# Kernel tuning notes

Measured on AMD Instinct MI355X. Metric: run time of the kernel, lower is better.

The kernel has to match this reference:

```python
import jax, jax.numpy as jnp
import numpy as np

B, T, D = 16, 2048, 384
BLOCK = 3
NB = D // BLOCK
EPS = 1e-8


def setup_inputs() -> dict:
    key = jax.random.key(0)
    ks = jax.random.split(key, 8)
    std = 0.02
    quat_sequence = jax.random.normal(ks[0], (B, T, 4), dtype=jnp.float32)
    # weights stored as (in, out); x @ W
    W_in = jax.random.normal(ks[1], (4, D), dtype=jnp.float32) * std
    W_biv = jax.random.normal(ks[2], (D, NB * 3), dtype=jnp.float32) * (1.0 / np.sqrt(D))
    b_biv = jnp.zeros((NB * 3,), dtype=jnp.float32)
    W_dec = jax.random.normal(ks[3], (D, D), dtype=jnp.float32) * (1.0 / np.sqrt(D))
    b_dec = jnp.full((D,), 1.4, dtype=jnp.float32)
    W_inj = jax.random.normal(ks[4], (D, D), dtype=jnp.float32) * (1.0 / np.sqrt(D))
    b_inj = jax.random.normal(ks[5], (D,), dtype=jnp.float32) * (1.0 / np.sqrt(D))
    W_out = jax.random.normal(ks[6], (D, 4), dtype=jnp.float32) * std
    return {
        'quat_sequence': quat_sequence,
        'W_in': W_in, 'W_biv': W_biv, 'b_biv': b_biv,
        'W_dec': W_dec, 'b_dec': b_dec, 'W_inj': W_inj, 'b_inj': b_inj,
        'W_out': W_out,
    }


def _quat_rotate_blocks(h_blocks, bivectors):
    # h_blocks, bivectors: (..., NB, 3)
    norm_b = jnp.clip(jnp.linalg.norm(bivectors, axis=-1, keepdims=True), EPS, None)
    half = norm_b / 2
    w = jnp.cos(half)[..., 0]
    s = (jnp.sin(half) / norm_b)[..., 0]
    qx = s * bivectors[..., 2]
    qy = -s * bivectors[..., 1]
    qz = s * bivectors[..., 0]
    vx, vy, vz = h_blocks[..., 0], h_blocks[..., 1], h_blocks[..., 2]
    tx = 2 * (qy * vz - qz * vy)
    ty = 2 * (qz * vx - qx * vz)
    tz = 2 * (qx * vy - qy * vx)
    rx = vx + w * tx + (qy * tz - qz * ty)
    ry = vy + w * ty + (qz * tx - qx * tz)
    rz = vz + w * tz + (qx * ty - qy * tx)
    return jnp.stack([rx, ry, rz], axis=-1)


def reference(quat_sequence, W_in, W_biv, b_biv, W_dec, b_dec, W_inj, b_inj, W_out):
    hidden_input = quat_sequence @ W_in                       # (B,T,D)
    bivectors_all = (hidden_input @ W_biv + b_biv).reshape(B, T, NB, 3)
    decay_all = jax.nn.sigmoid(hidden_input @ W_dec + b_dec)  # (B,T,D)
    injection_all = hidden_input @ W_inj + b_inj              # (B,T,D)

    def step(h, xs):
        biv, dec, inj = xs  # (B,NB,3), (B,D), (B,D)
        rot = _quat_rotate_blocks(h.reshape(B, NB, 3), biv).reshape(B, D)
        h_next = dec * rot + inj
        return h_next, h_next

    h0 = jnp.zeros((B, D), dtype=quat_sequence.dtype)
    xs = (jnp.swapaxes(bivectors_all, 0, 1),
          jnp.swapaxes(decay_all, 0, 1),
          jnp.swapaxes(injection_all, 0, 1))
    _, hidden_seq = jax.lax.scan(step, h0, xs)                # (T,B,D)
    hidden_output = jnp.swapaxes(hidden_seq, 0, 1)            # (B,T,D)

    predicted_raw = hidden_output @ W_out                     # (B,T,4)
    norm = jnp.clip(jnp.linalg.norm(predicted_raw, axis=-1, keepdims=True), EPS, None)
    return predicted_raw / norm
```

## Files before the change

kernel.cpp:

```cpp
#include <hip/hip_runtime.h>
#include <hip/hip_bf16.h>
#include <hip/hip_fp16.h>

#define BB 16
#define TT 2048
#define DD 384
#define GG 2048
#define CC 256
#define LL 8
#define HSTRIDE (DD + 8)
#define EPSF 1e-8f
#define RCPF(x) __builtin_amdgcn_rcpf(x)


__global__ __launch_bounds__(256) void precompute_wc(
        const float* __restrict__ W_in,
        const float* __restrict__ W_biv,
        const float* __restrict__ W_dec,
        const float* __restrict__ W_inj,
        const float* __restrict__ b_biv,
        const float* __restrict__ b_dec,
        const float* __restrict__ b_inj,
        float* __restrict__ Wc) {
    int m = blockIdx.x;
    int jl = threadIdx.x & 15;
    int dp = threadIdx.x >> 4;
    int j = blockIdx.y * 16 + jl;
    const float* __restrict__ W = (m == 0) ? W_biv : (m == 1) ? W_dec : W_inj;
    float a[4] = {0.f, 0.f, 0.f, 0.f};
    for (int d = dp; d < DD; d += 16) {
        float wv = W[d * DD + j];
#pragma unroll
        for (int k = 0; k < 4; ++k) a[k] = fmaf(W_in[k * DD + d], wv, a[k]);
    }
    __shared__ float red[16][17][4];
#pragma unroll
    for (int k = 0; k < 4; ++k) red[dp][jl][k] = a[k];
    __syncthreads();
    for (int s = 8; s >= 1; s >>= 1) {
        if (dp < s) {
#pragma unroll
            for (int k = 0; k < 4; ++k) red[dp][jl][k] += red[dp + s][jl][k];
        }
        __syncthreads();
    }
    int n = j / 3, comp = j - 3 * n;
    if (dp < 4) {
        Wc[((m * 4 + dp) * 128 + n) * 4 + comp] = red[0][jl][dp];
    } else if (dp == 4) {
#pragma unroll
        for (int k = 0; k < 4; ++k) Wc[((m * 4 + k) * 128 + n) * 4 + 3] = 0.f;
        Wc[(1536 + m * 128 + n) * 4 + 3] = 0.f;
    } else if (dp == 5) {
        const float* bsrc = (m == 0) ? b_biv : (m == 1) ? b_dec : b_inj;
        Wc[(1536 + m * 128 + n) * 4 + comp] = bsrc[j];
    }
}

struct Wts {
    float wb[4][3], wd[4][3], wi[4][3];
    float bb[3], bd[3], bj[3];
};

__device__ __forceinline__ void load_wts(const float4* __restrict__ Wc4, int n, Wts& W) {
#pragma unroll
    for (int k = 0; k < 4; ++k) {
        float4 v = Wc4[(0 * 4 + k) * 128 + n];
        W.wb[k][0] = v.x; W.wb[k][1] = v.y; W.wb[k][2] = v.z;
    }
#pragma unroll
    for (int k = 0; k < 4; ++k) {
        float4 v = Wc4[(1 * 4 + k) * 128 + n];
        W.wd[k][0] = v.x; W.wd[k][1] = v.y; W.wd[k][2] = v.z;
    }
#pragma unroll
    for (int k = 0; k < 4; ++k) {
        float4 v = Wc4[(2 * 4 + k) * 128 + n];
        W.wi[k][0] = v.x; W.wi[k][1] = v.y; W.wi[k][2] = v.z;
    }
    float4 b0 = Wc4[1536 + 0 * 128 + n];
    float4 b1 = Wc4[1536 + 1 * 128 + n];
    float4 b2 = Wc4[1536 + 2 * 128 + n];
    W.bb[0] = b0.x; W.bb[1] = b0.y; W.bb[2] = b0.z;
    W.bd[0] = b1.x; W.bd[1] = b1.y; W.bd[2] = b1.z;
    W.bj[0] = b2.x; W.bj[1] = b2.y; W.bj[2] = b2.z;
}

#define DOTW(M, c, bias) \
    fmaf(q.w, W.M[3][c], fmaf(q.z, W.M[2][c], fmaf(q.y, W.M[1][c], fmaf(q.x, W.M[0][c], bias))))

__device__ __forceinline__ void step_parts(const Wts& W, float4 q,
        float& dec0, float& dec1, float& dec2,
        float& w, float& qx, float& qy, float& qz,
        float& i0, float& i1, float& i2) {
    float bx = DOTW(wb, 0, W.bb[0]);
    float by = DOTW(wb, 1, W.bb[1]);
    float bz = DOTW(wb, 2, W.bb[2]);
    float d0 = DOTW(wd, 0, W.bd[0]);
    float d1 = DOTW(wd, 1, W.bd[1]);
    float d2 = DOTW(wd, 2, W.bd[2]);
    i0 = DOTW(wi, 0, W.bj[0]);
    i1 = DOTW(wi, 1, W.bj[1]);
    i2 = DOTW(wi, 2, W.bj[2]);
    dec0 = RCPF(1.f + __expf(-d0));
    dec1 = RCPF(1.f + __expf(-d1));
    dec2 = RCPF(1.f + __expf(-d2));
    float u = fmaf(bx, bx, fmaf(by, by, bz * bz));
    w = fmaf(u, fmaf(u, 2.6041667e-3f, -0.125f), 1.f);
    float s = fmaf(u, fmaf(u, 2.6041667e-4f, -2.0833333e-2f), 0.5f);
    qx = s * bz; qy = -s * by; qz = s * bx;
}

__device__ __forceinline__ void step_matrix(const Wts& W, float4 q,
                                            float M[9], float& i0, float& i1, float& i2) {
    float dec0, dec1, dec2, w, qx, qy, qz;
    step_parts(W, q, dec0, dec1, dec2, w, qx, qy, qz, i0, i1, i2);
    float xx = qx*qx, yy = qy*qy, zz = qz*qz;
    float xy = qx*qy, xz = qx*qz, yz = qy*qz;
    float wxs = w*qx, wys = w*qy, wzs = w*qz;
    M[0] = dec0 * (1.f - 2.f*(yy+zz));
    M[1] = dec0 * (2.f*(xy - wzs));
    M[2] = dec0 * (2.f*(xz + wys));
    M[3] = dec1 * (2.f*(xy + wzs));
    M[4] = dec1 * (1.f - 2.f*(xx+zz));
    M[5] = dec1 * (2.f*(yz - wxs));
    M[6] = dec2 * (2.f*(xz - wys));
    M[7] = dec2 * (2.f*(yz + wxs));
    M[8] = dec2 * (1.f - 2.f*(xx+yy));
}

__device__ __forceinline__ void step_init12(const Wts& W, float4 q, float A[12]) {
    float M[9], i0, i1, i2;
    step_matrix(W, q, M, i0, i1, i2);
#pragma unroll
    for (int e = 0; e < 9; ++e) A[e] = M[e];
    A[9] = i0; A[10] = i1; A[11] = i2;
}

__device__ __forceinline__ void step_compose12(const Wts& W, float4 q, float A[12]) {
    float M[9], i0, i1, i2;
    step_matrix(W, q, M, i0, i1, i2);
    float n0 = fmaf(M[0], A[0], fmaf(M[1], A[3], M[2] * A[6]));
    float n1 = fmaf(M[0], A[1], fmaf(M[1], A[4], M[2] * A[7]));
    float n2 = fmaf(M[0], A[2], fmaf(M[1], A[5], M[2] * A[8]));
    float n3 = fmaf(M[3], A[0], fmaf(M[4], A[3], M[5] * A[6]));
    float n4 = fmaf(M[3], A[1], fmaf(M[4], A[4], M[5] * A[7]));
    float n5 = fmaf(M[3], A[2], fmaf(M[4], A[5], M[5] * A[8]));
    float n6 = fmaf(M[6], A[0], fmaf(M[7], A[3], M[8] * A[6]));
    float n7 = fmaf(M[6], A[1], fmaf(M[7], A[4], M[8] * A[7]));
    float n8 = fmaf(M[6], A[2], fmaf(M[7], A[5], M[8] * A[8]));
    float n9  = fmaf(M[0], A[9], fmaf(M[1], A[10], fmaf(M[2], A[11], i0)));
    float n10 = fmaf(M[3], A[9], fmaf(M[4], A[10], fmaf(M[5], A[11], i1)));
    float n11 = fmaf(M[6], A[9], fmaf(M[7], A[10], fmaf(M[8], A[11], i2)));
    A[0]=n0; A[1]=n1; A[2]=n2; A[3]=n3; A[4]=n4; A[5]=n5;
    A[6]=n6; A[7]=n7; A[8]=n8; A[9]=n9; A[10]=n10; A[11]=n11;
}

__device__ __forceinline__ void step_apply(const Wts& W, float4 q,
                                           float& vx, float& vy, float& vz) {
    float dec0, dec1, dec2, w, qx, qy, qz, i0, i1, i2;
    step_parts(W, q, dec0, dec1, dec2, w, qx, qy, qz, i0, i1, i2);
    float tx = 2.f * (qy * vz - qz * vy);
    float ty = 2.f * (qz * vx - qx * vz);
    float tz = 2.f * (qx * vy - qy * vx);
    float rx = vx + w * tx + (qy * tz - qz * ty);
    float ry = vy + w * ty + (qz * tx - qx * tz);
    float rz = vz + w * tz + (qx * ty - qy * tx);
    vx = fmaf(dec0, rx, i0);
    vy = fmaf(dec1, ry, i1);
    vz = fmaf(dec2, rz, i2);
}

#define COMPOSE(R, C, P)                                                    \
    R[0] = fmaf(C[0], P[0], fmaf(C[1], P[3], C[2] * P[6]));                 \
    R[1] = fmaf(C[0], P[1], fmaf(C[1], P[4], C[2] * P[7]));                 \
    R[2] = fmaf(C[0], P[2], fmaf(C[1], P[5], C[2] * P[8]));                 \
    R[3] = fmaf(C[3], P[0], fmaf(C[4], P[3], C[5] * P[6]));                 \
    R[4] = fmaf(C[3], P[1], fmaf(C[4], P[4], C[5] * P[7]));                 \
    R[5] = fmaf(C[3], P[2], fmaf(C[4], P[5], C[5] * P[8]));                 \
    R[6] = fmaf(C[6], P[0], fmaf(C[7], P[3], C[8] * P[6]));                 \
    R[7] = fmaf(C[6], P[1], fmaf(C[7], P[4], C[8] * P[7]));                 \
    R[8] = fmaf(C[6], P[2], fmaf(C[7], P[5], C[8] * P[8]));                 \
    R[9]  = fmaf(C[0], P[9], fmaf(C[1], P[10], fmaf(C[2], P[11], C[9])));   \
    R[10] = fmaf(C[3], P[9], fmaf(C[4], P[10], fmaf(C[5], P[11], C[10])));  \
    R[11] = fmaf(C[6], P[9], fmaf(C[7], P[10], fmaf(C[8], P[11], C[11])));

__global__ __launch_bounds__(128) void chunk_compose(
        const float* __restrict__ quat,
        const float4* __restrict__ Wc4,
        float4* __restrict__ AffH) {
    int c = blockIdx.x, b = blockIdx.y, n = threadIdx.x;
    int g = b * 128 + n;

    const float4* __restrict__ qp = (const float4*)(quat + (size_t)b * TT * 4) + c * LL;
    float4 q[LL];
#pragma unroll
    for (int t = 0; t < LL; ++t) q[t] = qp[t];

    Wts W;
    load_wts(Wc4, n, W);

    float Alo[12], Ahi[12];
    step_init12(W, q[0], Alo);
    step_init12(W, q[LL / 2], Ahi);
#pragma unroll
    for (int t = 1; t < LL / 2; ++t) {
        step_compose12(W, q[t], Alo);
        step_compose12(W, q[LL / 2 + t], Ahi);
    }
    float A[12];
    COMPOSE(A, Ahi, Alo);

    union { __half2 h2[8]; float4 f4[2]; } u;
#pragma unroll
    for (int e = 0; e < 6; ++e) u.h2[e] = __floats2half2_rn(A[2 * e], A[2 * e + 1]);
    u.h2[6] = __floats2half2_rn(0.f, 0.f);
    u.h2[7] = __floats2half2_rn(0.f, 0.f);
    float4* o = AffH + ((size_t)c * GG + g) * 2;
    o[0] = u.f4[0];
    o[1] = u.f4[1];
}

__global__ __launch_bounds__(256) void chunk_scan(
        const float4* __restrict__ AffH,
        float4* __restrict__ Hs) {
    int g = (blockIdx.x * 256 + threadIdx.x) >> 6;
    int l = threadIdx.x & 63;

    float m[4][12];
#pragma unroll
    for (int k = 0; k < 4; ++k) {
        const float4* a = AffH + ((size_t)(4 * l + k) * GG + g) * 2;
        union { __half2 h2[8]; float4 f4[2]; } u;
        u.f4[0] = a[0]; u.f4[1] = a[1];
#pragma unroll
        for (int e = 0; e < 6; ++e) {
            float2 v = __half22float2(u.h2[e]);
            m[k][2 * e] = v.x; m[k][2 * e + 1] = v.y;
        }
    }
    float q01[12], q012[12], Q[12];
    COMPOSE(q01, m[1], m[0]);
    COMPOSE(q012, m[2], q01);
    COMPOSE(Q, m[3], q012);

    float P[12];
#pragma unroll
    for (int k = 0; k < 12; ++k) P[k] = __shfl_up(Q[k], 1);
    if (l == 0) {
        P[0]=1.f; P[1]=0.f; P[2]=0.f; P[3]=0.f; P[4]=1.f; P[5]=0.f;
        P[6]=0.f; P[7]=0.f; P[8]=1.f; P[9]=0.f; P[10]=0.f; P[11]=0.f;
    }
#pragma unroll
    for (int sft = 1; sft < 64; sft <<= 1) {
        float S[12], N[12];
#pragma unroll
        for (int k = 0; k < 12; ++k) S[k] = __shfl_up(P[k], sft);
        COMPOSE(N, P, S);
        bool act = (l >= sft);
#pragma unroll
        for (int k = 0; k < 12; ++k) P[k] = act ? N[k] : P[k];
    }

    float h0 = P[9], h1 = P[10], h2 = P[11];
#pragma unroll
    for (int k = 0; k < 4; ++k) {
        Hs[(size_t)(4 * l + k) * GG + g] = make_float4(h0, h1, h2, 0.f);
        if (k < 3) {
            float n0 = fmaf(m[k][0], h0, fmaf(m[k][1], h1, fmaf(m[k][2], h2, m[k][9])));
            float n1 = fmaf(m[k][3], h0, fmaf(m[k][4], h1, fmaf(m[k][5], h2, m[k][10])));
            float n2 = fmaf(m[k][6], h0, fmaf(m[k][7], h1, fmaf(m[k][8], h2, m[k][11])));
            h0 = n0; h1 = n1; h2 = n2;
        }
    }
}

__global__ __launch_bounds__(128) void chunk_apply_out(
        const float* __restrict__ quat,
        const float4* __restrict__ Wc4,
        const float* __restrict__ W_out,
        const float4* __restrict__ Hs,
        float* __restrict__ out) {
    int c = blockIdx.x, b = blockIdx.y, n = threadIdx.x;
    int g = b * 128 + n;

    const float4* __restrict__ qp = (const float4*)(quat + (size_t)b * TT * 4) + c * LL;
    float4 q[LL];
#pragma unroll
    for (int t = 0; t < LL; ++t) q[t] = qp[t];

    float4 h4 = Hs[(size_t)c * GG + g];

    Wts W;
    load_wts(Wc4, n, W);

    __shared__ float H[LL][HSTRIDE];

    int j0 = 3 * n;
    float vx = h4.x, vy = h4.y, vz = h4.z;
#pragma unroll
    for (int t = 0; t < LL; ++t) {
        step_apply(W, q[t], vx, vy, vz);
        H[t][j0] = vx; H[t][j0 + 1] = vy; H[t][j0 + 2] = vz;
    }
    __syncthreads();

    int r = n >> 4, p = n & 15;
    float s0 = 0.f, s1 = 0.f, s2 = 0.f, s3 = 0.f;
#pragma unroll 8
    for (int j = 0; j < DD / 16; ++j) {
        int d = p + 16 * j;
        float hv = H[r][d];
        float4 wv = *(const float4*)(W_out + (size_t)d * 4);
        s0 = fmaf(hv, wv.x, s0);
        s1 = fmaf(hv, wv.y, s1);
        s2 = fmaf(hv, wv.z, s2);
        s3 = fmaf(hv, wv.w, s3);
    }
#pragma unroll
    for (int off = 1; off <= 8; off <<= 1) {
        s0 += __shfl_xor(s0, off);
        s1 += __shfl_xor(s1, off);
        s2 += __shfl_xor(s2, off);
        s3 += __shfl_xor(s3, off);
    }
    if (p == 0) {
        float norm = fmaxf(sqrtf(fmaf(s0, s0, fmaf(s1, s1, fmaf(s2, s2, s3 * s3)))), EPSF);
        float inv = RCPF(norm);
        float* outp = out + ((size_t)b * TT + (size_t)c * LL + r) * 4;
        *(float4*)outp = make_float4(s0 * inv, s1 * inv, s2 * inv, s3 * inv);
    }
}

extern "C" void kernel_launch(void* const* d_in, const int* in_sizes, int n_in,
                              void* d_out, int out_size, void* d_ws, size_t ws_size,
                              hipStream_t stream) {
    const float* quat  = (const float*)d_in[0];
    const float* W_in  = (const float*)d_in[1];
    const float* W_biv = (const float*)d_in[2];
    const float* b_biv = (const float*)d_in[3];
    const float* W_dec = (const float*)d_in[4];
    const float* b_dec = (const float*)d_in[5];
    const float* W_inj = (const float*)d_in[6];
    const float* b_inj = (const float*)d_in[7];
    const float* W_out = (const float*)d_in[8];
    float* out = (float*)d_out;

    const size_t AFF_OFF = 32768;
    const size_t AFF_B   = (size_t)CC * GG * 32;
    const size_t HS_OFF  = AFF_OFF + AFF_B;

    float*  Wc   = (float*)d_ws;
    float4* Wc4  = (float4*)d_ws;
    float4* AffH = (float4*)((char*)d_ws + AFF_OFF);
    float4* Hs   = (float4*)((char*)d_ws + HS_OFF);

    precompute_wc<<<dim3(3, DD / 16), dim3(256), 0, stream>>>(
        W_in, W_biv, W_dec, W_inj, b_biv, b_dec, b_inj, Wc);
    chunk_compose<<<dim3(CC, BB), dim3(128), 0, stream>>>(quat, Wc4, AffH);
    chunk_scan<<<dim3(GG / 4), dim3(256), 0, stream>>>(AffH, Hs);
    chunk_apply_out<<<dim3(CC, BB), dim3(128), 0, stream>>>(quat, Wc4, W_out, Hs, out);
}
```

Before: 60.31 us.

## Split apply-phase recurrence into two parallel half-chains via stored half-chunk affine

chunk_compose now also stores the first half-chunk affine map (in fp16) to a new workspace buffer. chunk_apply_out loads it and computes the hidden state at the midpoint of the chunk directly, so the two 4-step halves of the 8-step recurrence run interleaved instead of as one 8-step dependent chain. This shortens the serial dependency chain and adds instruction-level parallelism, at the cost of an extra 32-byte write and read per thread-chunk and more fp16 rounding error at the midpoint.

```diff
diff --git a/kernel.cpp b/kernel.cpp
--- a/kernel.cpp
+++ b/kernel.cpp
@@ -185,10 +185,31 @@
     R[10] = fmaf(C[3], P[9], fmaf(C[4], P[10], fmaf(C[5], P[11], C[10])));  \
     R[11] = fmaf(C[6], P[9], fmaf(C[7], P[10], fmaf(C[8], P[11], C[11])));
 
+__device__ __forceinline__ void pack12(const float A[12], float4* dst) {
+    union { __half2 h2[8]; float4 f4[2]; } u;
+#pragma unroll
+    for (int e = 0; e < 6; ++e) u.h2[e] = __floats2half2_rn(A[2 * e], A[2 * e + 1]);
+    u.h2[6] = __floats2half2_rn(0.f, 0.f);
+    u.h2[7] = __floats2half2_rn(0.f, 0.f);
+    dst[0] = u.f4[0];
+    dst[1] = u.f4[1];
+}
+
+__device__ __forceinline__ void unpack12(const float4* src, float A[12]) {
+    union { __half2 h2[8]; float4 f4[2]; } u;
+    u.f4[0] = src[0]; u.f4[1] = src[1];
+#pragma unroll
+    for (int e = 0; e < 6; ++e) {
+        float2 v = __half22float2(u.h2[e]);
+        A[2 * e] = v.x; A[2 * e + 1] = v.y;
+    }
+}
+
 __global__ __launch_bounds__(128) void chunk_compose(
         const float* __restrict__ quat,
         const float4* __restrict__ Wc4,
-        float4* __restrict__ AffH) {
+        float4* __restrict__ AffH,
+        float4* __restrict__ AffLo) {
     int c = blockIdx.x, b = blockIdx.y, n = threadIdx.x;
     int g = b * 128 + n;
 
@@ -208,17 +229,10 @@
         step_compose12(W, q[t], Alo);
         step_compose12(W, q[LL / 2 + t], Ahi);
     }
+    pack12(Alo, AffLo + ((size_t)c * GG + g) * 2);
     float A[12];
     COMPOSE(A, Ahi, Alo);
-
-    union { __half2 h2[8]; float4 f4[2]; } u;
-#pragma unroll
-    for (int e = 0; e < 6; ++e) u.h2[e] = __floats2half2_rn(A[2 * e], A[2 * e + 1]);
-    u.h2[6] = __floats2half2_rn(0.f, 0.f);
-    u.h2[7] = __floats2half2_rn(0.f, 0.f);
-    float4* o = AffH + ((size_t)c * GG + g) * 2;
-    o[0] = u.f4[0];
-    o[1] = u.f4[1];
+    pack12(A, AffH + ((size_t)c * GG + g) * 2);
 }
 
 __global__ __launch_bounds__(256) void chunk_scan(
@@ -229,16 +243,9 @@
 
     float m[4][12];
 #pragma unroll
-    for (int k = 0; k < 4; ++k) {
-        const float4* a = AffH + ((size_t)(4 * l + k) * GG + g) * 2;
-        union { __half2 h2[8]; float4 f4[2]; } u;
-        u.f4[0] = a[0]; u.f4[1] = a[1];
-#pragma unroll
-        for (int e = 0; e < 6; ++e) {
-            float2 v = __half22float2(u.h2[e]);
-            m[k][2 * e] = v.x; m[k][2 * e + 1] = v.y;
-        }
-    }
+    for (int k = 0; k < 4; ++k)
+        unpack12(AffH + ((size_t)(4 * l + k) * GG + g) * 2, m[k]);
+
     float q01[12], q012[12], Q[12];
     COMPOSE(q01, m[1], m[0]);
     COMPOSE(q012, m[2], q01);
@@ -280,6 +287,7 @@
         const float4* __restrict__ Wc4,
         const float* __restrict__ W_out,
         const float4* __restrict__ Hs,
+        const float4* __restrict__ AffLo,
         float* __restrict__ out) {
     int c = blockIdx.x, b = blockIdx.y, n = threadIdx.x;
     int g = b * 128 + n;
@@ -290,6 +298,8 @@
     for (int t = 0; t < LL; ++t) q[t] = qp[t];
 
     float4 h4 = Hs[(size_t)c * GG + g];
+    float alo[12];
+    unpack12(AffLo + ((size_t)c * GG + g) * 2, alo);
 
     Wts W;
     load_wts(Wc4, n, W);
@@ -297,11 +307,17 @@
     __shared__ float H[LL][HSTRIDE];
 
     int j0 = 3 * n;
-    float vx = h4.x, vy = h4.y, vz = h4.z;
-#pragma unroll
-    for (int t = 0; t < LL; ++t) {
-        step_apply(W, q[t], vx, vy, vz);
-        H[t][j0] = vx; H[t][j0 + 1] = vy; H[t][j0 + 2] = vz;
+    float ax = h4.x, ay = h4.y, az = h4.z;
+    float bx = fmaf(alo[0], ax, fmaf(alo[1], ay, fmaf(alo[2], az, alo[9])));
+    float by = fmaf(alo[3], ax, fmaf(alo[4], ay, fmaf(alo[5], az, alo[10])));
+    float bz = fmaf(alo[6], ax, fmaf(alo[7], ay, fmaf(alo[8], az, alo[11])));
+
+#pragma unroll
+    for (int t = 0; t < LL / 2; ++t) {
+        step_apply(W, q[t], ax, ay, az);
+        step_apply(W, q[LL / 2 + t], bx, by, bz);
+        H[t][j0] = ax; H[t][j0 + 1] = ay; H[t][j0 + 2] = az;
+        H[LL / 2 + t][j0] = bx; H[LL / 2 + t][j0 + 1] = by; H[LL / 2 + t][j0 + 2] = bz;
     }
     __syncthreads();
 
@@ -348,16 +364,18 @@
 
     const size_t AFF_OFF = 32768;
     const size_t AFF_B   = (size_t)CC * GG * 32;
-    const size_t HS_OFF  = AFF_OFF + AFF_B;
-
-    float*  Wc   = (float*)d_ws;
-    float4* Wc4  = (float4*)d_ws;
-    float4* AffH = (float4*)((char*)d_ws + AFF_OFF);
-    float4* Hs   = (float4*)((char*)d_ws + HS_OFF);
+    const size_t ALO_OFF = AFF_OFF + AFF_B;
+    const size_t HS_OFF  = ALO_OFF + AFF_B;
+
+    float*  Wc    = (float*)d_ws;
+    float4* Wc4   = (float4*)d_ws;
+    float4* AffH  = (float4*)((char*)d_ws + AFF_OFF);
+    float4* AffLo = (float4*)((char*)d_ws + ALO_OFF);
+    float4* Hs    = (float4*)((char*)d_ws + HS_OFF);
 
     precompute_wc<<<dim3(3, DD / 16), dim3(256), 0, stream>>>(
         W_in, W_biv, W_dec, W_inj, b_biv, b_dec, b_inj, Wc);
-    chunk_compose<<<dim3(CC, BB), dim3(128), 0, stream>>>(quat, Wc4, AffH);
+    chunk_compose<<<dim3(CC, BB), dim3(128), 0, stream>>>(quat, Wc4, AffH, AffLo);
     chunk_scan<<<dim3(GG / 4), dim3(256), 0, stream>>>(AffH, Hs);
-    chunk_apply_out<<<dim3(CC, BB), dim3(128), 0, stream>>>(quat, Wc4, W_out, Hs, out);
-}
+    chunk_apply_out<<<dim3(CC, BB), dim3(128), 0, stream>>>(quat, Wc4, W_out, Hs, AffLo, out);
+}
```

Result: faster. 58.69 us (-2.7%).
